# Performance work log

Hardware: AMD Instinct MI355X
Metric: run time of the kernel (lower is better)

## Reference

```python
import jax, jax.numpy as jnp
import numpy as np

N_HEAD_HALF = 8          # config.n_head // 2
LAMBDA_INIT = 0.2        # diff_lambda_init
RMS_EPS = 1.1920929e-07  # torch.finfo(float32).eps (F.rms_norm default)
ROPE_BASE = 10000.0


def setup_inputs() -> dict:
    key = jax.random.key(0)
    ks = jax.random.split(key, 9)
    B, T, C = 2, 2048, 2048
    HD = C // N_HEAD_HALF  # 256
    s = 0.02
    return {
        "x": jax.random.normal(ks[0], (B, T, C), jnp.float32),
        "wq": jax.random.normal(ks[1], (C, C), jnp.float32) * s,
        "wk": jax.random.normal(ks[2], (C, C), jnp.float32) * s,
        "wv": jax.random.normal(ks[3], (C, C), jnp.float32) * s,
        "wo": jax.random.normal(ks[4], (C, C), jnp.float32) * s,
        "lq1": jax.random.normal(ks[5], (HD,), jnp.float32) * 0.1,
        "lk1": jax.random.normal(ks[6], (HD,), jnp.float32) * 0.1,
        "lq2": jax.random.normal(ks[7], (HD,), jnp.float32) * 0.1,
        "lk2": jax.random.normal(ks[8], (HD,), jnp.float32) * 0.1,
    }


def _rms_norm(x):
    var = jnp.mean(x * x, axis=-1, keepdims=True)
    return x * jax.lax.rsqrt(var + RMS_EPS)


def _rotary(x):
    # Faithful to original bug: positions run along axis 1 (the HEAD axis),
    # since Rotary is applied after transpose(1,2). x: (B, NH, T, D)
    d = x.shape[-1]
    inv_freq = (1.0 / ROPE_BASE) ** (jnp.arange(0, d, 2, dtype=jnp.float32) / d)
    t = jnp.arange(x.shape[1], dtype=jnp.float32)
    freqs = jnp.outer(t, inv_freq)                      # (NH, d/2)
    cos = jnp.cos(freqs)[None, :, None, :]
    sin = jnp.sin(freqs)[None, :, None, :]
    x1, x2 = jnp.split(x, 2, axis=-1)
    return jnp.concatenate((x1 * cos + x2 * sin, -x1 * sin + x2 * cos), axis=-1)


def _causal_attn(q, k, v, scale):
    # q,k: (B,NH,T,Dh)  v: (B,NH,T,HD)
    T = q.shape[2]
    s = jnp.einsum("bhqd,bhkd->bhqk", q, k) * scale
    mask = jnp.tril(jnp.ones((T, T), dtype=bool))
    s = jnp.where(mask, s, jnp.float32(-jnp.inf))
    p = jax.nn.softmax(s, axis=-1)
    return jnp.einsum("bhqk,bhkd->bhqd", p, v)


def reference(x, wq, wk, wv, wo, lq1, lk1, lq2, lk2):
    B, T, C = x.shape
    NH = N_HEAD_HALF
    HD = C // NH
    HH = HD // 2

    lam1 = jnp.exp(jnp.sum(lq1 * lk1))
    lam2 = jnp.exp(jnp.sum(lq2 * lk2))
    lam = lam1 - lam2 + LAMBDA_INIT

    q = (x @ wq.T).reshape(B, T, NH, 2, HH).transpose(0, 2, 1, 3, 4)
    k = (x @ wk.T).reshape(B, T, NH, 2, HH).transpose(0, 2, 1, 3, 4)
    v = (x @ wv.T).reshape(B, T, NH, HD).transpose(0, 2, 1, 3)

    q1 = _rotary(_rms_norm(q[..., 0, :]))
    q2 = _rotary(_rms_norm(q[..., 1, :]))
    k1 = _rotary(_rms_norm(k[..., 0, :]))
    k2 = _rotary(_rms_norm(k[..., 1, :]))

    scale = 1.0 / jnp.sqrt(jnp.float32(HH))
    y = _causal_attn(q1, k1, v, scale) - lam * _causal_attn(q2, k2, v, scale)

    y = y.transpose(0, 2, 1, 3).reshape(B, T, C)
    y = (y @ wo.T) * (1.0 - LAMBDA_INIT)
    return y
```

## Files before the change

### kernel.cpp

```cpp
#include <hip/hip_runtime.h>
#include <hip/hip_bf16.h>

using bf16 = __hip_bfloat16;
typedef __bf16 bf16x8_t __attribute__((ext_vector_type(8)));
typedef __bf16 bf16x4_t __attribute__((ext_vector_type(4)));
typedef float f32x4  __attribute__((ext_vector_type(4)));
typedef float f32x16 __attribute__((ext_vector_type(16)));

#define AS1 __attribute__((address_space(1)))
#define AS3 __attribute__((address_space(3)))

__device__ __forceinline__ void gll16(const void* g, void* l) {
  __builtin_amdgcn_global_load_lds((const AS1 void*)g, (AS3 void*)l, 16u, 0, 0u);
}

__device__ __forceinline__ __bf16 tobf(float f) {
  bf16 h = __float2bfloat16(f);
  return __builtin_bit_cast(__bf16, h);
}

__global__ __launch_bounds__(256) void k_cvt(
    const float* __restrict__ x,  const float* __restrict__ wq,
    const float* __restrict__ wk, const float* __restrict__ wv,
    const float* __restrict__ wo,
    bf16* __restrict__ xb,  bf16* __restrict__ wqb, bf16* __restrict__ wkb,
    bf16* __restrict__ wvb, bf16* __restrict__ wob) {
  size_t id = (size_t)blockIdx.x * 256 + threadIdx.x;
  const float* s; bf16* d; size_t off;
  if (id < 2097152) { s = x; d = xb; off = id; }
  else {
    size_t r = id - 2097152;
    unsigned w = (unsigned)(r >> 20);
    off = r & 1048575u;
    s = (w == 0) ? wq : (w == 1) ? wk : (w == 2) ? wv : wo;
    d = (w == 0) ? wqb : (w == 1) ? wkb : (w == 2) ? wvb : wob;
  }
  const float4 v = ((const float4*)s)[off];
  bf16x4_t o = { tobf(v.x), tobf(v.y), tobf(v.z), tobf(v.w) };
  *(bf16x4_t*)(d + off * 4) = o;
}

__global__ __launch_bounds__(256) void k_lam(
    const float* __restrict__ lq1, const float* __restrict__ lk1,
    const float* __restrict__ lq2, const float* __restrict__ lk2,
    float* __restrict__ lam) {
  __shared__ float r1[4], r2[4];
  int t = threadIdx.x;
  float a = lq1[t] * lk1[t];
  float b = lq2[t] * lk2[t];
#pragma unroll
  for (int s = 1; s < 64; s <<= 1) { a += __shfl_xor(a, s); b += __shfl_xor(b, s); }
  if ((t & 63) == 0) { r1[t >> 6] = a; r2[t >> 6] = b; }
  __syncthreads();
  if (t == 0) {
    float s1 = r1[0] + r1[1] + r1[2] + r1[3];
    float s2 = r2[0] + r2[1] + r2[2] + r2[3];
    *lam = expf(s1) - expf(s2) + 0.2f;
  }
}

#define MFMA16(a, b, c) __builtin_amdgcn_mfma_f32_16x16x32_bf16(a, b, c, 0, 0, 0)

template<bool SWAP>
__device__ __forceinline__ void gemm256(
    const bf16* __restrict__ A, const bf16* __restrict__ B,
    int m0, int n0, bf16* lds, f32x4 (&acc)[8][4]) {
  const int tid = threadIdx.x, lane = tid & 63;
  const int wave = tid >> 6, m = wave >> 2, n = wave & 3;
  const int g = lane >> 4, l15 = lane & 15, l7 = lane & 7;

  const int sid0 = tid, sid1 = tid + 512;
  const int sr0 = sid0 >> 3, sc0 = (sid0 & 7) ^ (sr0 & 7);
  const int sr1 = sid1 >> 3, sc1 = (sid1 & 7) ^ (sr1 & 7);

  auto stageA = [&](int t, int h) {
    bf16* d = lds + ((size_t)((t & 1) * 2 + h)) * 8192;
    gll16(A + (size_t)(m0 + h * 128 + sr0) * 2048 + t * 64 + sc0 * 8, d + sid0 * 8);
    gll16(A + (size_t)(m0 + h * 128 + sr1) * 2048 + t * 64 + sc1 * 8, d + sid1 * 8);
  };
  auto stageB = [&](int t, int h) {
    bf16* d = lds + 32768 + ((size_t)((t & 1) * 2 + h)) * 8192;
    gll16(B + (size_t)(n0 + h * 128 + sr0) * 2048 + t * 64 + sc0 * 8, d + sid0 * 8);
    gll16(B + (size_t)(n0 + h * 128 + sr1) * 2048 + t * 64 + sc1 * 8, d + sid1 * 8);
  };

  stageA(0, 0); stageB(0, 0); stageB(0, 1); stageA(0, 1);
  stageA(1, 0); stageB(1, 0); stageB(1, 1);
  asm volatile("s_waitcnt vmcnt(6)\n\ts_barrier" ::: "memory");

  for (int t = 0; t < 32; ++t) {
    const bf16* lA0 = lds + ((size_t)((t & 1) * 2 + 0)) * 8192;
    const bf16* lA1 = lds + ((size_t)((t & 1) * 2 + 1)) * 8192;
    const bf16* lB0 = lds + 32768 + ((size_t)((t & 1) * 2 + 0)) * 8192;
    const bf16* lB1 = lds + 32768 + ((size_t)((t & 1) * 2 + 1)) * 8192;
    bf16x8_t afl[4][2], afh[4][2], bvl[2][2], bvh[2][2];

#pragma unroll
    for (int ks = 0; ks < 2; ++ks) {
      const int pc = ((ks * 4 + g) ^ l7) * 8;
#pragma unroll
      for (int rf = 0; rf < 4; ++rf)
        afl[rf][ks] = *(const bf16x8_t*)(lA0 + (m * 64 + rf * 16 + l15) * 64 + pc);
#pragma unroll
      for (int cf = 0; cf < 2; ++cf)
        bvl[cf][ks] = *(const bf16x8_t*)(lB0 + (cf * 64 + n * 16 + l15) * 64 + pc);
    }
    if (t + 1 < 32) stageA(t + 1, 1);
    asm volatile("s_barrier" ::: "memory");
    __builtin_amdgcn_s_setprio(1);
#pragma unroll
    for (int ks = 0; ks < 2; ++ks)
#pragma unroll
      for (int rf = 0; rf < 4; ++rf)
#pragma unroll
        for (int cf = 0; cf < 2; ++cf)
          acc[rf][cf] = SWAP ? MFMA16(bvl[cf][ks], afl[rf][ks], acc[rf][cf])
                             : MFMA16(afl[rf][ks], bvl[cf][ks], acc[rf][cf]);
    __builtin_amdgcn_s_setprio(0);
    asm volatile("s_barrier" ::: "memory");

#pragma unroll
    for (int ks = 0; ks < 2; ++ks) {
      const int pc = ((ks * 4 + g) ^ l7) * 8;
#pragma unroll
      for (int cf = 0; cf < 2; ++cf)
        bvh[cf][ks] = *(const bf16x8_t*)(lB1 + (cf * 64 + n * 16 + l15) * 64 + pc);
    }
    if (t + 2 < 32) stageA(t + 2, 0);
    asm volatile("s_barrier" ::: "memory");
    __builtin_amdgcn_s_setprio(1);
#pragma unroll
    for (int ks = 0; ks < 2; ++ks)
#pragma unroll
      for (int rf = 0; rf < 4; ++rf)
#pragma unroll
        for (int cf = 0; cf < 2; ++cf)
          acc[rf][cf + 2] = SWAP ? MFMA16(bvh[cf][ks], afl[rf][ks], acc[rf][cf + 2])
                                 : MFMA16(afl[rf][ks], bvh[cf][ks], acc[rf][cf + 2]);
    __builtin_amdgcn_s_setprio(0);
    asm volatile("s_barrier" ::: "memory");

#pragma unroll
    for (int ks = 0; ks < 2; ++ks) {
      const int pc = ((ks * 4 + g) ^ l7) * 8;
#pragma unroll
      for (int rf = 0; rf < 4; ++rf)
        afh[rf][ks] = *(const bf16x8_t*)(lA1 + (m * 64 + rf * 16 + l15) * 64 + pc);
    }
    if (t + 2 < 32) stageB(t + 2, 0);
    asm volatile("s_barrier" ::: "memory");
    __builtin_amdgcn_s_setprio(1);
#pragma unroll
    for (int ks = 0; ks < 2; ++ks)
#pragma unroll
      for (int rf = 0; rf < 4; ++rf)
#pragma unroll
        for (int cf = 0; cf < 2; ++cf)
          acc[rf + 4][cf + 2] = SWAP ? MFMA16(bvh[cf][ks], afh[rf][ks], acc[rf + 4][cf + 2])
                                     : MFMA16(afh[rf][ks], bvh[cf][ks], acc[rf + 4][cf + 2]);
    __builtin_amdgcn_s_setprio(0);
    asm volatile("s_barrier" ::: "memory");

    if (t + 2 < 32) stageB(t + 2, 1);
    asm volatile("s_barrier" ::: "memory");
    __builtin_amdgcn_s_setprio(1);
#pragma unroll
    for (int ks = 0; ks < 2; ++ks)
#pragma unroll
      for (int rf = 0; rf < 4; ++rf)
#pragma unroll
        for (int cf = 0; cf < 2; ++cf)
          acc[rf + 4][cf] = SWAP ? MFMA16(bvl[cf][ks], afh[rf][ks], acc[rf + 4][cf])
                                 : MFMA16(afh[rf][ks], bvl[cf][ks], acc[rf + 4][cf]);
    __builtin_amdgcn_s_setprio(0);
    if (t < 30)      asm volatile("s_waitcnt vmcnt(6)\n\ts_barrier" ::: "memory");
    else             asm volatile("s_waitcnt vmcnt(0)\n\ts_barrier" ::: "memory");
  }
}

__global__ __launch_bounds__(512, 2) void k_gemm_qkv(
    const bf16* __restrict__ xb,
    const bf16* __restrict__ wqb, const bf16* __restrict__ wkb,
    const bf16* __restrict__ wvb,
    bf16* __restrict__ q1, bf16* __restrict__ q2,
    bf16* __restrict__ k1, bf16* __restrict__ k2,
    bf16* __restrict__ vt) {
  __shared__ __align__(16) bf16 lds[65536];
  __shared__ float exs[2][4][256];
  __shared__ float lCs[64], lSn[64];
  const int z  = blockIdx.z;
  const int m0 = blockIdx.y * 256, n0 = blockIdx.x * 256;
  const int nh = blockIdx.x;
  const int tid = threadIdx.x, lane = tid & 63, wave = tid >> 6;
  const int m = wave >> 2, n = wave & 3;
  const int g = lane >> 4, l15 = lane & 15;
  f32x4 acc[8][4] = {};

  if (z < 2) {
    if (tid < 64) {
      float fr = exp2f(-(float)tid * 0.20762050593045951f);
      float sn, cs;
      sincosf((float)nh * fr, &sn, &cs);
      lCs[tid] = cs; lSn[tid] = sn;
    }
    const bf16* Bm = z ? wkb : wqb;
    gemm256<true>(xb, Bm, m0, n0, lds, acc);

#pragma unroll
    for (int rf = 0; rf < 8; ++rf) {
      float s0 = 0.f, s1 = 0.f;
#pragma unroll
      for (int r = 0; r < 4; ++r) {
        s0 += acc[rf][0][r] * acc[rf][0][r] + acc[rf][1][r] * acc[rf][1][r];
        s1 += acc[rf][2][r] * acc[rf][2][r] + acc[rf][3][r] * acc[rf][3][r];
      }
      s0 += __shfl_xor(s0, 16); s0 += __shfl_xor(s0, 32);
      s1 += __shfl_xor(s1, 16); s1 += __shfl_xor(s1, 32);
      const int rrow = (rf >> 2) * 128 + m * 64 + (rf & 3) * 16 + l15;
      if (g == 0) { exs[0][n][rrow] = s0; exs[1][n][rrow] = s1; }
    }
    __syncthreads();
    bf16* dst1 = z ? k1 : q1;
    bf16* dst2 = z ? k2 : q2;
    const int j = n * 16 + 4 * g;
#pragma unroll
    for (int rf = 0; rf < 8; ++rf) {
      const int rrow = (rf >> 2) * 128 + m * 64 + (rf & 3) * 16 + l15;
      const float t0 = exs[0][0][rrow] + exs[0][1][rrow] + exs[0][2][rrow] + exs[0][3][rrow];
      const float t1 = exs[1][0][rrow] + exs[1][1][rrow] + exs[1][2][rrow] + exs[1][3][rrow];
      const float inv0 = rsqrtf(t0 * (1.0f / 128.0f) + 1.1920929e-07f);
      const float inv1 = rsqrtf(t1 * (1.0f / 128.0f) + 1.1920929e-07f);
      const size_t base = ((size_t)(m0 + rrow) * 8 + nh) * 128;
      bf16x4_t o1a, o2a, o1b, o2b;
#pragma unroll
      for (int r = 0; r < 4; ++r) {
        const float cs = lCs[j + r], sn = lSn[j + r];
        float x1 = acc[rf][0][r] * inv0, x2 = acc[rf][1][r] * inv0;
        o1a[r] = tobf(x1 * cs + x2 * sn);
        o2a[r] = tobf(x2 * cs - x1 * sn);
        x1 = acc[rf][2][r] * inv1; x2 = acc[rf][3][r] * inv1;
        o1b[r] = tobf(x1 * cs + x2 * sn);
        o2b[r] = tobf(x2 * cs - x1 * sn);
      }
      *(bf16x4_t*)(dst1 + base + j)      = o1a;
      *(bf16x4_t*)(dst1 + base + j + 64) = o2a;
      *(bf16x4_t*)(dst2 + base + j)      = o1b;
      *(bf16x4_t*)(dst2 + base + j + 64) = o2b;
    }
  } else {
    gemm256<false>(xb, wvb, m0, n0, lds, acc);
#pragma unroll
    for (int rf = 0; rf < 8; ++rf)
#pragma unroll
      for (int cf = 0; cf < 4; ++cf) {
        const int rb = m0 + (rf >> 2) * 128 + m * 64 + (rf & 3) * 16 + 4 * g;
        const int hd = (cf & 1) * 64 + (cf >> 1) * 128 + n * 16 + l15;
        const int b = rb >> 11, t = rb & 2047;
        bf16x4_t pv;
#pragma unroll
        for (int r = 0; r < 4; ++r) pv[r] = tobf(acc[rf][cf][r]);
        *(bf16x4_t*)(vt + ((size_t)((b * 8 + nh) * 256 + hd)) * 2048 + t) = pv;
      }
  }
}

template<bool SWAP>
__device__ __forceinline__ void gemm_core(
    const bf16* __restrict__ A, const bf16* __restrict__ Bm,
    int m0, int n0, bf16* lA, bf16* lB, f32x4 (&acc)[4][4]) {
  const int tid  = threadIdx.x;
  const int lane = tid & 63;
  const int g    = lane >> 4;
  const int l15  = lane & 15;
  const int l7   = lane & 7;
  const int wave = tid >> 6;
  const int wm   = (wave >> 1) * 64;
  const int wn   = (wave & 1) * 64;

  int srow[4], ssc[4];
#pragma unroll
  for (int j = 0; j < 4; ++j) {
    int id = tid + j * 256;
    srow[j] = id >> 3;
    ssc[j]  = (id & 7) ^ (srow[j] & 7);
  }

  for (int k0 = 0; k0 < 2048; k0 += 64) {
    __syncthreads();
#pragma unroll
    for (int j = 0; j < 4; ++j) {
      int id = tid + j * 256;
      gll16(A  + (size_t)(m0 + srow[j]) * 2048 + k0 + ssc[j] * 8, lA + id * 8);
      gll16(Bm + (size_t)(n0 + srow[j]) * 2048 + k0 + ssc[j] * 8, lB + id * 8);
    }
    __syncthreads();
#pragma unroll
    for (int ks = 0; ks < 2; ++ks) {
      const int pc = (ks * 4 + g) ^ l7;
      bf16x8_t af[4], bfr[4];
#pragma unroll
      for (int mt = 0; mt < 4; ++mt)
        af[mt] = *(const bf16x8_t*)(lA + (wm + mt * 16 + l15) * 64 + pc * 8);
#pragma unroll
      for (int nt = 0; nt < 4; ++nt)
        bfr[nt] = *(const bf16x8_t*)(lB + (wn + nt * 16 + l15) * 64 + pc * 8);
#pragma unroll
      for (int mt = 0; mt < 4; ++mt)
#pragma unroll
        for (int nt = 0; nt < 4; ++nt) {
          if (SWAP)
            acc[mt][nt] = MFMA16(bfr[nt], af[mt], acc[mt][nt]);
          else
            acc[mt][nt] = MFMA16(af[mt], bfr[nt], acc[mt][nt]);
        }
    }
  }
}

__global__ __launch_bounds__(256) void k_gemm_out(
    const bf16* __restrict__ yb, const bf16* __restrict__ wob,
    float* __restrict__ outp) {
  __shared__ __align__(16) bf16 lA[128 * 64];
  __shared__ __align__(16) bf16 lB[128 * 64];
  const int m0 = blockIdx.y * 128, n0 = blockIdx.x * 128;
  f32x4 acc[4][4] = {};
  gemm_core<true>(yb, wob, m0, n0, lA, lB, acc);
  const int lane = threadIdx.x & 63, wave = threadIdx.x >> 6;
  const int g = lane >> 4, l15 = lane & 15;
  const int wm = (wave >> 1) * 64, wn = (wave & 1) * 64;
#pragma unroll
  for (int mt = 0; mt < 4; ++mt)
#pragma unroll
    for (int nt = 0; nt < 4; ++nt) {
      int row = m0 + wm + mt * 16 + l15;
      int col = n0 + wn + nt * 16 + 4 * g;
      f32x4 v;
#pragma unroll
      for (int r = 0; r < 4; ++r) v[r] = acc[mt][nt][r] * 0.8f;
      *(f32x4*)(outp + (size_t)row * 2048 + col) = v;
    }
}

__global__ __launch_bounds__(512, 2) void k_flash(
    const bf16* __restrict__ q1b, const bf16* __restrict__ q2b,
    const bf16* __restrict__ k1b, const bf16* __restrict__ k2b,
    const bf16* __restrict__ vtb, const float* __restrict__ lamp,
    bf16* __restrict__ yb) {
  __shared__ __align__(16) bf16 smem[65536];
  __shared__ float mx[8][32], lx[8][32];
  const int tid  = threadIdx.x;
  const int lane = tid & 63, wave = tid >> 6;
  const int pair = blockIdx.x;
  const int bh = blockIdx.y;
  const int b = bh >> 3, nh = bh & 7;
  const int at = wave & 1, qg = (wave >> 1) & 1, kvh = wave >> 2;
  const int l31 = lane & 31, g5 = lane >> 5, l7 = lane & 7;
  const float sl2e = 0.12751743f;
  const float lam = *lamp;

  auto stage = [&](int kt, int buf) {
    bf16* dst = smem + buf * 32768;
    const int k0 = kt * 64;
#pragma unroll
    for (int it = 0; it < 2; ++it) {
      int id = tid + it * 512;
      int row = id >> 4, c = id & 15;
      int sc = (c & 8) | ((c & 7) ^ (row & 7));
      size_t goff = ((size_t)(b * 2048 + k0 + row) * 8 + nh) * 128 + sc * 8;
      gll16(k1b + goff, dst + id * 8);
      gll16(k2b + goff, dst + 8192 + id * 8);
    }
#pragma unroll
    for (int it = 0; it < 4; ++it) {
      int id = tid + it * 512;
      int row = id >> 3, c = id & 7;
      int sc = c ^ (row & 7);
      gll16(vtb + ((size_t)(bh * 256 + row)) * 2048 + k0 + sc * 8,
            dst + 16384 + id * 8);
    }
  };

  bf16x8_t qf[8];
  auto loadQ = [&](int qt) {
    int qglob = qt * 64 + qg * 32 + l31;
    const bf16* qp = (at ? q2b : q1b) +
                     ((size_t)(b * 2048 + qglob) * 8 + nh) * 128 + g5 * 8;
#pragma unroll
    for (int ks = 0; ks < 8; ++ks) qf[ks] = *(const bf16x8_t*)(qp + ks * 16);
  };

  f32x16 O[8];
  float mrun, lrun;
  auto resetO = [&]() {
#pragma unroll
    for (int i = 0; i < 8; ++i)
#pragma unroll
      for (int j = 0; j < 16; ++j) O[i][j] = 0.f;
    mrun = -1e30f; lrun = 0.f;
  };

  auto step = [&](int kt, int buf, int qt) {
    const int k0 = kt * 64 + kvh * 32;
    if (k0 > qt * 64 + qg * 32 + 31) return;
    const bf16* lk = smem + buf * 32768 + (at ? 8192 : 0);
    const bf16* lv = smem + buf * 32768 + 16384;
    const int qglob = qt * 64 + qg * 32 + l31;

    f32x16 s0;
#pragma unroll
    for (int j = 0; j < 16; ++j) s0[j] = 0.f;
#pragma unroll
    for (int ks = 0; ks < 8; ++ks) {
      int cl = ks * 2 + g5;
      int pc = (cl & 8) | ((cl & 7) ^ l7);
      bf16x8_t a0 = *(const bf16x8_t*)(lk + (kvh * 32 + l31) * 128 + pc * 8);
      s0 = __builtin_amdgcn_mfma_f32_32x32x16_bf16(a0, qf[ks], s0, 0, 0, 0);
    }

    const bool needmask = (k0 + 31 > qt * 64 + qg * 32);
    float rmax = -3.0e38f;
#pragma unroll
    for (int r = 0; r < 16; ++r) {
      float v0 = s0[r] * sl2e;
      if (needmask) {
        int key0 = k0 + (r & 3) + 8 * (r >> 2) + 4 * g5;
        if (key0 > qglob) v0 = -1e30f;
      }
      s0[r] = v0;
      rmax = fmaxf(rmax, v0);
    }
    rmax = fmaxf(rmax, __shfl_xor(rmax, 32));
    if (!__all(rmax - mrun <= 8.0f)) {
      float mnew = fmaxf(mrun, rmax);
      float alpha = exp2f(mrun - mnew);
      lrun *= alpha;
#pragma unroll
      for (int i = 0; i < 8; ++i) O[i] *= alpha;
      mrun = mnew;
    }
    float psum = 0.f;
#pragma unroll
    for (int r = 0; r < 16; ++r) {
      float p0 = exp2f(s0[r] - mrun);
      s0[r] = p0;
      psum += p0;
    }
    psum += __shfl_xor(psum, 32);
    lrun += psum;

#pragma unroll
    for (int sl = 0; sl < 2; ++sl) {
      bf16x4_t lo, hi;
#pragma unroll
      for (int j = 0; j < 4; ++j) {
        lo[j] = tobf(s0[sl * 8 + j]);
        hi[j] = tobf(s0[sl * 8 + 4 + j]);
      }
      bf16x4_t send = g5 ? lo : hi;
      int2 si = __builtin_bit_cast(int2, send);
      int2 ri;
      ri.x = __shfl_xor(si.x, 32);
      ri.y = __shfl_xor(si.y, 32);
      bf16x4_t recv = __builtin_bit_cast(bf16x4_t, ri);
      bf16x4_t f0 = g5 ? recv : lo;
      bf16x4_t f1 = g5 ? hi : recv;
      bf16x8_t pf = { f0[0], f0[1], f0[2], f0[3], f1[0], f1[1], f1[2], f1[3] };

      const int cl = kvh * 4 + sl * 2 + g5;
#pragma unroll
      for (int mt = 0; mt < 8; ++mt) {
        bf16x8_t vf = *(const bf16x8_t*)(lv + (mt * 32 + l31) * 64 + (cl ^ l7) * 8);
        O[mt] = __builtin_amdgcn_mfma_f32_32x32x16_bf16(vf, pf, O[mt], 0, 0, 0);
      }
    }
  };

  auto finish = [&](int qt, bf16* cbuf) {
    const int qglob = qt * 64 + qg * 32 + l31;
    float* XF = (float*)cbuf;
    __syncthreads();
    if (g5 == 0) { mx[wave][l31] = mrun; lx[wave][l31] = lrun; }
    __syncthreads();
    const float mo  = mx[wave ^ 4][l31];
    const float lo2 = lx[wave ^ 4][l31];
    const float ms = fmaxf(mrun, mo);
    const float ws = exp2f(mrun - ms);
    const float wo = exp2f(mo - ms);
    const float lstar = lrun * ws + lo2 * wo;
#pragma unroll
    for (int rnd = 0; rnd < 2; ++rnd) {
      if (at == rnd && kvh == 1) {
#pragma unroll
        for (int mt = 0; mt < 8; ++mt)
#pragma unroll
          for (int rq = 0; rq < 4; ++rq) {
            int hd = mt * 32 + 8 * rq + 4 * g5;
            f32x4 v;
#pragma unroll
            for (int i = 0; i < 4; ++i) v[i] = O[mt][rq * 4 + i] * ws;
            *(f32x4*)(XF + qg * 8192 + l31 * 256 + hd) = v;
          }
      }
      __syncthreads();
      if (at == rnd && kvh == 0) {
#pragma unroll
        for (int mt = 0; mt < 8; ++mt)
#pragma unroll
          for (int rq = 0; rq < 4; ++rq) {
            int hd = mt * 32 + 8 * rq + 4 * g5;
            f32x4 v = *(const f32x4*)(XF + qg * 8192 + l31 * 256 + hd);
#pragma unroll
            for (int i = 0; i < 4; ++i)
              O[mt][rq * 4 + i] = O[mt][rq * 4 + i] * ws + v[i];
          }
      }
      __syncthreads();
    }
    const float invl = 1.f / lstar;
    if (kvh == 0 && at == 1) {
      const float f = lam * invl;
#pragma unroll
      for (int mt = 0; mt < 8; ++mt)
#pragma unroll
        for (int rq = 0; rq < 4; ++rq) {
          int hd = mt * 32 + 8 * rq + 4 * g5;
          bf16x4_t pv;
#pragma unroll
          for (int i = 0; i < 4; ++i) pv[i] = tobf(O[mt][rq * 4 + i] * f);
          *(bf16x4_t*)(cbuf + (size_t)(qg * 32 + l31) * 264 + hd) = pv;
        }
    }
    __syncthreads();
    if (kvh == 0 && at == 0) {
#pragma unroll
      for (int mt = 0; mt < 8; ++mt)
#pragma unroll
        for (int rq = 0; rq < 4; ++rq) {
          int hd = mt * 32 + 8 * rq + 4 * g5;
          bf16x4_t o2 = *(const bf16x4_t*)(cbuf + (size_t)(qg * 32 + l31) * 264 + hd);
          bf16x4_t pv;
#pragma unroll
          for (int i = 0; i < 4; ++i)
            pv[i] = tobf(O[mt][rq * 4 + i] * invl - (float)o2[i]);
          *(bf16x4_t*)(yb + (size_t)(b * 2048 + qglob) * 2048 + nh * 256 + hd) = pv;
        }
    }
  };

  const int qtB = 31 - pair, qtA = pair;

  loadQ(qtB);
  resetO();
  stage(0, 0);
  for (int kt = 0; kt <= qtB; ++kt) {
    __syncthreads();
    if (kt < qtB) stage(kt + 1, (kt + 1) & 1);
    else          stage(0, (kt + 1) & 1);
    step(kt, kt & 1, qtB);
  }
  finish(qtB, smem + (qtB & 1) * 32768);

  loadQ(qtA);
  resetO();
  for (int kt = 0; kt <= qtA; ++kt) {
    __syncthreads();
    if (kt < qtA) stage(kt + 1, (qtB + kt + 2) & 1);
    step(kt, (qtB + 1 + kt) & 1, qtA);
  }
  finish(qtA, smem + 32768);
}

extern "C" void kernel_launch(void* const* d_in, const int* in_sizes, int n_in,
                              void* d_out, int out_size, void* d_ws, size_t ws_size,
                              hipStream_t stream) {
  (void)in_sizes; (void)n_in; (void)out_size; (void)ws_size;
  const float* x   = (const float*)d_in[0];
  const float* wq  = (const float*)d_in[1];
  const float* wk  = (const float*)d_in[2];
  const float* wv  = (const float*)d_in[3];
  const float* wo  = (const float*)d_in[4];
  const float* lq1 = (const float*)d_in[5];
  const float* lk1 = (const float*)d_in[6];
  const float* lq2 = (const float*)d_in[7];
  const float* lk2 = (const float*)d_in[8];
  float* out = (float*)d_out;

  char* p = (char*)d_ws;
  float* lam = (float*)p;            p += 256;
  bf16* xb  = (bf16*)p;              p += (size_t)4096 * 2048 * 2;
  bf16* wqb = (bf16*)p;              p += (size_t)2048 * 2048 * 2;
  bf16* wkb = (bf16*)p;              p += (size_t)2048 * 2048 * 2;
  bf16* wvb = (bf16*)p;              p += (size_t)2048 * 2048 * 2;
  bf16* wob = (bf16*)p;              p += (size_t)2048 * 2048 * 2;
  bf16* vt  = (bf16*)p;              p += (size_t)4096 * 2048 * 2;
  bf16* q1b = (bf16*)p;              p += (size_t)4096 * 1024 * 2;
  bf16* q2b = (bf16*)p;              p += (size_t)4096 * 1024 * 2;
  bf16* k1b = (bf16*)p;              p += (size_t)4096 * 1024 * 2;
  bf16* k2b = (bf16*)p;              p += (size_t)4096 * 1024 * 2;
  bf16* yb  = (bf16*)p;              p += (size_t)4096 * 2048 * 2;

  k_cvt<<<24576, 256, 0, stream>>>(x, wq, wk, wv, wo, xb, wqb, wkb, wvb, wob);
  k_lam<<<1, 256, 0, stream>>>(lq1, lk1, lq2, lk2, lam);
  k_gemm_qkv<<<dim3(8, 16, 3), 512, 0, stream>>>(xb, wqb, wkb, wvb,
                                                 q1b, q2b, k1b, k2b, vt);
  k_flash<<<dim3(16, 16), 512, 0, stream>>>(q1b, q2b, k1b, k2b, vt, lam, yb);
  k_gemm_out<<<dim3(16, 32), 256, 0, stream>>>(yb, wob, out);
}
```

Measured before the change: 425.7 us.

## Retile GEMMs to 256x128 with triple-buffered LDS pipeline and fuse lambda kernel

Replaces the 256x256 double-buffered QKV GEMM with a shared 256x128 tile GEMM that keeps three LDS stages and prefetches two k-steps ahead, doubling the QKV grid. The output projection, which used a simple 128x128 single-buffered GEMM, now uses the same pipelined 256x128 path. The lambda reduction moves into an extra block of the conversion kernel to drop one launch. The epilogue's RMS norm now sums across two waves through shared memory. The aim is more blocks in flight and better latency hiding, at the cost of less reuse per tile.

```diff
diff --git a/kernel.cpp b/kernel.cpp
--- a/kernel.cpp
+++ b/kernel.cpp
@@ -23,8 +23,26 @@
     const float* __restrict__ x,  const float* __restrict__ wq,
     const float* __restrict__ wk, const float* __restrict__ wv,
     const float* __restrict__ wo,
+    const float* __restrict__ lq1, const float* __restrict__ lk1,
+    const float* __restrict__ lq2, const float* __restrict__ lk2,
     bf16* __restrict__ xb,  bf16* __restrict__ wqb, bf16* __restrict__ wkb,
-    bf16* __restrict__ wvb, bf16* __restrict__ wob) {
+    bf16* __restrict__ wvb, bf16* __restrict__ wob, float* __restrict__ lam) {
+  if (blockIdx.x == 24576) {
+    __shared__ float r1[4], r2[4];
+    int t = threadIdx.x;
+    float a = lq1[t] * lk1[t];
+    float b = lq2[t] * lk2[t];
+#pragma unroll
+    for (int s = 1; s < 64; s <<= 1) { a += __shfl_xor(a, s); b += __shfl_xor(b, s); }
+    if ((t & 63) == 0) { r1[t >> 6] = a; r2[t >> 6] = b; }
+    __syncthreads();
+    if (t == 0) {
+      float s1 = r1[0] + r1[1] + r1[2] + r1[3];
+      float s2 = r2[0] + r2[1] + r2[2] + r2[3];
+      *lam = expf(s1) - expf(s2) + 0.2f;
+    }
+    return;
+  }
   size_t id = (size_t)blockIdx.x * 256 + threadIdx.x;
   const float* s; bf16* d; size_t off;
   if (id < 2097152) { s = x; d = xb; off = id; }
@@ -40,72 +58,82 @@
   *(bf16x4_t*)(d + off * 4) = o;
 }
 
-__global__ __launch_bounds__(256) void k_lam(
-    const float* __restrict__ lq1, const float* __restrict__ lk1,
-    const float* __restrict__ lq2, const float* __restrict__ lk2,
-    float* __restrict__ lam) {
-  __shared__ float r1[4], r2[4];
-  int t = threadIdx.x;
-  float a = lq1[t] * lk1[t];
-  float b = lq2[t] * lk2[t];
-#pragma unroll
-  for (int s = 1; s < 64; s <<= 1) { a += __shfl_xor(a, s); b += __shfl_xor(b, s); }
-  if ((t & 63) == 0) { r1[t >> 6] = a; r2[t >> 6] = b; }
-  __syncthreads();
-  if (t == 0) {
-    float s1 = r1[0] + r1[1] + r1[2] + r1[3];
-    float s2 = r2[0] + r2[1] + r2[2] + r2[3];
-    *lam = expf(s1) - expf(s2) + 0.2f;
-  }
-}
-
 #define MFMA16(a, b, c) __builtin_amdgcn_mfma_f32_16x16x32_bf16(a, b, c, 0, 0, 0)
 
 template<bool SWAP>
-__device__ __forceinline__ void gemm256(
+__device__ __forceinline__ void gemmKS(
     const bf16* __restrict__ A, const bf16* __restrict__ B,
-    int m0, int n0, bf16* lds, f32x4 (&acc)[8][4]) {
+    int m0, int n0, bf16* lA_, bf16* lB_, f32x4 (&acc)[4][4]) {
   const int tid = threadIdx.x, lane = tid & 63;
-  const int wave = tid >> 6, m = wave >> 2, n = wave & 3;
+  const int wave = tid >> 6, m = wave >> 1, n = wave & 1;
   const int g = lane >> 4, l15 = lane & 15, l7 = lane & 7;
 
-  const int sid0 = tid, sid1 = tid + 512;
-  const int sr0 = sid0 >> 3, sc0 = (sid0 & 7) ^ (sr0 & 7);
-  const int sr1 = sid1 >> 3, sc1 = (sid1 & 7) ^ (sr1 & 7);
-
-  auto stageA = [&](int t, int h) {
-    bf16* d = lds + ((size_t)((t & 1) * 2 + h)) * 8192;
-    gll16(A + (size_t)(m0 + h * 128 + sr0) * 2048 + t * 64 + sc0 * 8, d + sid0 * 8);
-    gll16(A + (size_t)(m0 + h * 128 + sr1) * 2048 + t * 64 + sc1 * 8, d + sid1 * 8);
-  };
-  auto stageB = [&](int t, int h) {
-    bf16* d = lds + 32768 + ((size_t)((t & 1) * 2 + h)) * 8192;
-    gll16(B + (size_t)(n0 + h * 128 + sr0) * 2048 + t * 64 + sc0 * 8, d + sid0 * 8);
-    gll16(B + (size_t)(n0 + h * 128 + sr1) * 2048 + t * 64 + sc1 * 8, d + sid1 * 8);
-  };
-
-  stageA(0, 0); stageB(0, 0); stageB(0, 1); stageA(0, 1);
-  stageA(1, 0); stageB(1, 0); stageB(1, 1);
+  auto stageA = [&](int t, int sl) {
+    bf16* d = lA_ + sl * 16384;
+#pragma unroll
+    for (int j = 0; j < 4; ++j) {
+      int id = tid + j * 512;
+      int row = id >> 3, sc = (id & 7) ^ (row & 7);
+      gll16(A + (size_t)(m0 + row) * 2048 + t * 64 + sc * 8, d + id * 8);
+    }
+  };
+  auto stageB = [&](int t, int sl) {
+    bf16* d = lB_ + sl * 8192;
+#pragma unroll
+    for (int j = 0; j < 2; ++j) {
+      int id = tid + j * 512;
+      int row = id >> 3, sc = (id & 7) ^ (row & 7);
+      gll16(B + (size_t)(n0 + row) * 2048 + t * 64 + sc * 8, d + id * 8);
+    }
+  };
+
+  stageA(0, 0); stageB(0, 0); stageA(1, 1); stageB(1, 1);
   asm volatile("s_waitcnt vmcnt(6)\n\ts_barrier" ::: "memory");
 
+  int s = 0;
   for (int t = 0; t < 32; ++t) {
-    const bf16* lA0 = lds + ((size_t)((t & 1) * 2 + 0)) * 8192;
-    const bf16* lA1 = lds + ((size_t)((t & 1) * 2 + 1)) * 8192;
-    const bf16* lB0 = lds + 32768 + ((size_t)((t & 1) * 2 + 0)) * 8192;
-    const bf16* lB1 = lds + 32768 + ((size_t)((t & 1) * 2 + 1)) * 8192;
-    bf16x8_t afl[4][2], afh[4][2], bvl[2][2], bvh[2][2];
+    const bf16* la = lA_ + s * 16384;
+    const bf16* lb = lB_ + s * 8192;
+    int sp = s + 2; if (sp >= 3) sp -= 3;
+    bf16x8_t af[4][2], bv[4][2];
 
 #pragma unroll
     for (int ks = 0; ks < 2; ++ks) {
       const int pc = ((ks * 4 + g) ^ l7) * 8;
 #pragma unroll
       for (int rf = 0; rf < 4; ++rf)
-        afl[rf][ks] = *(const bf16x8_t*)(lA0 + (m * 64 + rf * 16 + l15) * 64 + pc);
+        af[rf][ks] = *(const bf16x8_t*)(la + (m * 64 + rf * 16 + l15) * 64 + pc);
 #pragma unroll
       for (int cf = 0; cf < 2; ++cf)
-        bvl[cf][ks] = *(const bf16x8_t*)(lB0 + (cf * 64 + n * 16 + l15) * 64 + pc);
-    }
-    if (t + 1 < 32) stageA(t + 1, 1);
+        bv[cf][ks] = *(const bf16x8_t*)(lb + (n * 32 + cf * 16 + l15) * 64 + pc);
+    }
+    if (t + 2 < 32) stageA(t + 2, sp);
+    asm volatile("s_barrier" ::: "memory");
+#pragma unroll
+    for (int ks = 0; ks < 2; ++ks) {
+      const int pc = ((ks * 4 + g) ^ l7) * 8;
+#pragma unroll
+      for (int cf = 0; cf < 2; ++cf)
+        bv[cf + 2][ks] =
+            *(const bf16x8_t*)(lb + (n * 32 + cf * 16 + 64 + l15) * 64 + pc);
+    }
+    __builtin_amdgcn_s_setprio(1);
+#pragma unroll
+    for (int ks = 0; ks < 2; ++ks)
+#pragma unroll
+      for (int rf = 0; rf < 4; ++rf)
+#pragma unroll
+        for (int cf = 0; cf < 2; ++cf)
+          acc[rf][cf] = SWAP ? MFMA16(bv[cf][ks], af[rf][ks], acc[rf][cf])
+                             : MFMA16(af[rf][ks], bv[cf][ks], acc[rf][cf]);
+    __builtin_amdgcn_s_setprio(0);
+
+    if (t + 2 < 32) {
+      stageB(t + 2, sp);
+      asm volatile("s_waitcnt vmcnt(6)" ::: "memory");
+    } else if (t == 30) {
+      asm volatile("s_waitcnt vmcnt(0)" ::: "memory");
+    }
     asm volatile("s_barrier" ::: "memory");
     __builtin_amdgcn_s_setprio(1);
 #pragma unroll
@@ -114,67 +142,10 @@
       for (int rf = 0; rf < 4; ++rf)
 #pragma unroll
         for (int cf = 0; cf < 2; ++cf)
-          acc[rf][cf] = SWAP ? MFMA16(bvl[cf][ks], afl[rf][ks], acc[rf][cf])
-                             : MFMA16(afl[rf][ks], bvl[cf][ks], acc[rf][cf]);
+          acc[rf][cf + 2] = SWAP ? MFMA16(bv[cf + 2][ks], af[rf][ks], acc[rf][cf + 2])
+                                 : MFMA16(af[rf][ks], bv[cf + 2][ks], acc[rf][cf + 2]);
     __builtin_amdgcn_s_setprio(0);
-    asm volatile("s_barrier" ::: "memory");
-
-#pragma unroll
-    for (int ks = 0; ks < 2; ++ks) {
-      const int pc = ((ks * 4 + g) ^ l7) * 8;
-#pragma unroll
-      for (int cf = 0; cf < 2; ++cf)
-        bvh[cf][ks] = *(const bf16x8_t*)(lB1 + (cf * 64 + n * 16 + l15) * 64 + pc);
-    }
-    if (t + 2 < 32) stageA(t + 2, 0);
-    asm volatile("s_barrier" ::: "memory");
-    __builtin_amdgcn_s_setprio(1);
-#pragma unroll
-    for (int ks = 0; ks < 2; ++ks)
-#pragma unroll
-      for (int rf = 0; rf < 4; ++rf)
-#pragma unroll
-        for (int cf = 0; cf < 2; ++cf)
-          acc[rf][cf + 2] = SWAP ? MFMA16(bvh[cf][ks], afl[rf][ks], acc[rf][cf + 2])
-                                 : MFMA16(afl[rf][ks], bvh[cf][ks], acc[rf][cf + 2]);
-    __builtin_amdgcn_s_setprio(0);
-    asm volatile("s_barrier" ::: "memory");
-
-#pragma unroll
-    for (int ks = 0; ks < 2; ++ks) {
-      const int pc = ((ks * 4 + g) ^ l7) * 8;
-#pragma unroll
-      for (int rf = 0; rf < 4; ++rf)
-        afh[rf][ks] = *(const bf16x8_t*)(lA1 + (m * 64 + rf * 16 + l15) * 64 + pc);
-    }
-    if (t + 2 < 32) stageB(t + 2, 0);
-    asm volatile("s_barrier" ::: "memory");
-    __builtin_amdgcn_s_setprio(1);
-#pragma unroll
-    for (int ks = 0; ks < 2; ++ks)
-#pragma unroll
-      for (int rf = 0; rf < 4; ++rf)
-#pragma unroll
-        for (int cf = 0; cf < 2; ++cf)
-          acc[rf + 4][cf + 2] = SWAP ? MFMA16(bvh[cf][ks], afh[rf][ks], acc[rf + 4][cf + 2])
-                                     : MFMA16(afh[rf][ks], bvh[cf][ks], acc[rf + 4][cf + 2]);
-    __builtin_amdgcn_s_setprio(0);
-    asm volatile("s_barrier" ::: "memory");
-
-    if (t + 2 < 32) stageB(t + 2, 1);
-    asm volatile("s_barrier" ::: "memory");
-    __builtin_amdgcn_s_setprio(1);
-#pragma unroll
-    for (int ks = 0; ks < 2; ++ks)
-#pragma unroll
-      for (int rf = 0; rf < 4; ++rf)
-#pragma unroll
-        for (int cf = 0; cf < 2; ++cf)
-          acc[rf + 4][cf] = SWAP ? MFMA16(bvl[cf][ks], afh[rf][ks], acc[rf + 4][cf])
-                                 : MFMA16(afh[rf][ks], bvl[cf][ks], acc[rf + 4][cf]);
-    __builtin_amdgcn_s_setprio(0);
-    if (t < 30)      asm volatile("s_waitcnt vmcnt(6)\n\ts_barrier" ::: "memory");
-    else             asm volatile("s_waitcnt vmcnt(0)\n\ts_barrier" ::: "memory");
+    s = (s == 2) ? 0 : s + 1;
   }
 }
 
@@ -185,16 +156,17 @@
     bf16* __restrict__ q1, bf16* __restrict__ q2,
     bf16* __restrict__ k1, bf16* __restrict__ k2,
     bf16* __restrict__ vt) {
-  __shared__ __align__(16) bf16 lds[65536];
-  __shared__ float exs[2][4][256];
+  __shared__ __align__(16) bf16 lA[3 * 16384];
+  __shared__ __align__(16) bf16 lB[3 * 8192];
+  __shared__ float exs[2][256];
   __shared__ float lCs[64], lSn[64];
   const int z  = blockIdx.z;
-  const int m0 = blockIdx.y * 256, n0 = blockIdx.x * 256;
-  const int nh = blockIdx.x;
+  const int m0 = blockIdx.y * 256, n0 = blockIdx.x * 128;
+  const int nh = blockIdx.x >> 1, p = blockIdx.x & 1;
   const int tid = threadIdx.x, lane = tid & 63, wave = tid >> 6;
-  const int m = wave >> 2, n = wave & 3;
+  const int m = wave >> 1, n = wave & 1;
   const int g = lane >> 4, l15 = lane & 15;
-  f32x4 acc[8][4] = {};
+  f32x4 acc[4][4] = {};
 
   if (z < 2) {
     if (tid < 64) {
@@ -204,57 +176,54 @@
       lCs[tid] = cs; lSn[tid] = sn;
     }
     const bf16* Bm = z ? wkb : wqb;
-    gemm256<true>(xb, Bm, m0, n0, lds, acc);
-
-#pragma unroll
-    for (int rf = 0; rf < 8; ++rf) {
-      float s0 = 0.f, s1 = 0.f;
-#pragma unroll
-      for (int r = 0; r < 4; ++r) {
-        s0 += acc[rf][0][r] * acc[rf][0][r] + acc[rf][1][r] * acc[rf][1][r];
-        s1 += acc[rf][2][r] * acc[rf][2][r] + acc[rf][3][r] * acc[rf][3][r];
-      }
-      s0 += __shfl_xor(s0, 16); s0 += __shfl_xor(s0, 32);
-      s1 += __shfl_xor(s1, 16); s1 += __shfl_xor(s1, 32);
-      const int rrow = (rf >> 2) * 128 + m * 64 + (rf & 3) * 16 + l15;
-      if (g == 0) { exs[0][n][rrow] = s0; exs[1][n][rrow] = s1; }
-    }
-    __syncthreads();
-    bf16* dst1 = z ? k1 : q1;
-    bf16* dst2 = z ? k2 : q2;
-    const int j = n * 16 + 4 * g;
-#pragma unroll
-    for (int rf = 0; rf < 8; ++rf) {
-      const int rrow = (rf >> 2) * 128 + m * 64 + (rf & 3) * 16 + l15;
-      const float t0 = exs[0][0][rrow] + exs[0][1][rrow] + exs[0][2][rrow] + exs[0][3][rrow];
-      const float t1 = exs[1][0][rrow] + exs[1][1][rrow] + exs[1][2][rrow] + exs[1][3][rrow];
-      const float inv0 = rsqrtf(t0 * (1.0f / 128.0f) + 1.1920929e-07f);
-      const float inv1 = rsqrtf(t1 * (1.0f / 128.0f) + 1.1920929e-07f);
+    gemmKS<true>(xb, Bm, m0, n0, lA, lB, acc);
+
+    float ssr[4];
+#pragma unroll
+    for (int rf = 0; rf < 4; ++rf) {
+      float ss = 0.f;
+#pragma unroll
+      for (int cf = 0; cf < 4; ++cf)
+#pragma unroll
+        for (int r = 0; r < 4; ++r) ss += acc[rf][cf][r] * acc[rf][cf][r];
+      ss += __shfl_xor(ss, 16);
+      ss += __shfl_xor(ss, 32);
+      ssr[rf] = ss;
+      if (g == 0) exs[n][m * 64 + rf * 16 + l15] = ss;
+    }
+    __syncthreads();
+    bf16* dst = z ? (p ? k2 : k1) : (p ? q2 : q1);
+#pragma unroll
+    for (int rf = 0; rf < 4; ++rf) {
+      const int rrow = m * 64 + rf * 16 + l15;
+      const float tt = ssr[rf] + exs[n ^ 1][rrow];
+      const float inv = rsqrtf(tt * (1.0f / 128.0f) + 1.1920929e-07f);
       const size_t base = ((size_t)(m0 + rrow) * 8 + nh) * 128;
-      bf16x4_t o1a, o2a, o1b, o2b;
-#pragma unroll
-      for (int r = 0; r < 4; ++r) {
-        const float cs = lCs[j + r], sn = lSn[j + r];
-        float x1 = acc[rf][0][r] * inv0, x2 = acc[rf][1][r] * inv0;
-        o1a[r] = tobf(x1 * cs + x2 * sn);
-        o2a[r] = tobf(x2 * cs - x1 * sn);
-        x1 = acc[rf][2][r] * inv1; x2 = acc[rf][3][r] * inv1;
-        o1b[r] = tobf(x1 * cs + x2 * sn);
-        o2b[r] = tobf(x2 * cs - x1 * sn);
-      }
-      *(bf16x4_t*)(dst1 + base + j)      = o1a;
-      *(bf16x4_t*)(dst1 + base + j + 64) = o2a;
-      *(bf16x4_t*)(dst2 + base + j)      = o1b;
-      *(bf16x4_t*)(dst2 + base + j + 64) = o2b;
+#pragma unroll
+      for (int cf = 0; cf < 2; ++cf) {
+        const int jb = n * 32 + cf * 16 + 4 * g;
+        bf16x4_t o1v, o2v;
+#pragma unroll
+        for (int r = 0; r < 4; ++r) {
+          const float cs = lCs[jb + r], sn = lSn[jb + r];
+          float x1 = acc[rf][cf][r] * inv;
+          float x2 = acc[rf][cf + 2][r] * inv;
+          o1v[r] = tobf(x1 * cs + x2 * sn);
+          o2v[r] = tobf(x2 * cs - x1 * sn);
+        }
+        *(bf16x4_t*)(dst + base + jb)      = o1v;
+        *(bf16x4_t*)(dst + base + jb + 64) = o2v;
+      }
     }
   } else {
-    gemm256<false>(xb, wvb, m0, n0, lds, acc);
-#pragma unroll
-    for (int rf = 0; rf < 8; ++rf)
+    gemmKS<false>(xb, wvb, m0, n0, lA, lB, acc);
+#pragma unroll
+    for (int rf = 0; rf < 4; ++rf)
 #pragma unroll
       for (int cf = 0; cf < 4; ++cf) {
-        const int rb = m0 + (rf >> 2) * 128 + m * 64 + (rf & 3) * 16 + 4 * g;
-        const int hd = (cf & 1) * 64 + (cf >> 1) * 128 + n * 16 + l15;
+        const int rb = m0 + m * 64 + rf * 16 + 4 * g;
+        const int col = n0 + n * 32 + (cf & 1) * 16 + (cf >> 1) * 64 + l15;
+        const int hd = col & 255;
         const int b = rb >> 11, t = rb & 2047;
         bf16x4_t pv;
 #pragma unroll
@@ -264,79 +233,26 @@
   }
 }
 
-template<bool SWAP>
-__device__ __forceinline__ void gemm_core(
-    const bf16* __restrict__ A, const bf16* __restrict__ Bm,
-    int m0, int n0, bf16* lA, bf16* lB, f32x4 (&acc)[4][4]) {
-  const int tid  = threadIdx.x;
-  const int lane = tid & 63;
-  const int g    = lane >> 4;
-  const int l15  = lane & 15;
-  const int l7   = lane & 7;
-  const int wave = tid >> 6;
-  const int wm   = (wave >> 1) * 64;
-  const int wn   = (wave & 1) * 64;
-
-  int srow[4], ssc[4];
-#pragma unroll
-  for (int j = 0; j < 4; ++j) {
-    int id = tid + j * 256;
-    srow[j] = id >> 3;
-    ssc[j]  = (id & 7) ^ (srow[j] & 7);
-  }
-
-  for (int k0 = 0; k0 < 2048; k0 += 64) {
-    __syncthreads();
-#pragma unroll
-    for (int j = 0; j < 4; ++j) {
-      int id = tid + j * 256;
-      gll16(A  + (size_t)(m0 + srow[j]) * 2048 + k0 + ssc[j] * 8, lA + id * 8);
-      gll16(Bm + (size_t)(n0 + srow[j]) * 2048 + k0 + ssc[j] * 8, lB + id * 8);
-    }
-    __syncthreads();
-#pragma unroll
-    for (int ks = 0; ks < 2; ++ks) {
-      const int pc = (ks * 4 + g) ^ l7;
-      bf16x8_t af[4], bfr[4];
-#pragma unroll
-      for (int mt = 0; mt < 4; ++mt)
-        af[mt] = *(const bf16x8_t*)(lA + (wm + mt * 16 + l15) * 64 + pc * 8);
-#pragma unroll
-      for (int nt = 0; nt < 4; ++nt)
-        bfr[nt] = *(const bf16x8_t*)(lB + (wn + nt * 16 + l15) * 64 + pc * 8);
-#pragma unroll
-      for (int mt = 0; mt < 4; ++mt)
-#pragma unroll
-        for (int nt = 0; nt < 4; ++nt) {
-          if (SWAP)
-            acc[mt][nt] = MFMA16(bfr[nt], af[mt], acc[mt][nt]);
-          else
-            acc[mt][nt] = MFMA16(af[mt], bfr[nt], acc[mt][nt]);
-        }
-    }
-  }
-}
-
-__global__ __launch_bounds__(256) void k_gemm_out(
+__global__ __launch_bounds__(512, 2) void k_gemm_out(
     const bf16* __restrict__ yb, const bf16* __restrict__ wob,
     float* __restrict__ outp) {
-  __shared__ __align__(16) bf16 lA[128 * 64];
-  __shared__ __align__(16) bf16 lB[128 * 64];
-  const int m0 = blockIdx.y * 128, n0 = blockIdx.x * 128;
+  __shared__ __align__(16) bf16 lA[3 * 16384];
+  __shared__ __align__(16) bf16 lB[3 * 8192];
+  const int m0 = blockIdx.y * 256, n0 = blockIdx.x * 128;
+  const int tid = threadIdx.x, lane = tid & 63, wave = tid >> 6;
+  const int m = wave >> 1, n = wave & 1;
+  const int g = lane >> 4, l15 = lane & 15;
   f32x4 acc[4][4] = {};
-  gemm_core<true>(yb, wob, m0, n0, lA, lB, acc);
-  const int lane = threadIdx.x & 63, wave = threadIdx.x >> 6;
-  const int g = lane >> 4, l15 = lane & 15;
-  const int wm = (wave >> 1) * 64, wn = (wave & 1) * 64;
-#pragma unroll
-  for (int mt = 0; mt < 4; ++mt)
-#pragma unroll
-    for (int nt = 0; nt < 4; ++nt) {
-      int row = m0 + wm + mt * 16 + l15;
-      int col = n0 + wn + nt * 16 + 4 * g;
+  gemmKS<true>(yb, wob, m0, n0, lA, lB, acc);
+#pragma unroll
+  for (int rf = 0; rf < 4; ++rf)
+#pragma unroll
+    for (int cf = 0; cf < 4; ++cf) {
+      const int row = m0 + m * 64 + rf * 16 + l15;
+      const int col = n0 + n * 32 + (cf & 1) * 16 + (cf >> 1) * 64 + 4 * g;
       f32x4 v;
 #pragma unroll
-      for (int r = 0; r < 4; ++r) v[r] = acc[mt][nt][r] * 0.8f;
+      for (int r = 0; r < 4; ++r) v[r] = acc[rf][cf][r] * 0.8f;
       *(f32x4*)(outp + (size_t)row * 2048 + col) = v;
     }
 }
@@ -599,10 +515,10 @@
   bf16* k2b = (bf16*)p;              p += (size_t)4096 * 1024 * 2;
   bf16* yb  = (bf16*)p;              p += (size_t)4096 * 2048 * 2;
 
-  k_cvt<<<24576, 256, 0, stream>>>(x, wq, wk, wv, wo, xb, wqb, wkb, wvb, wob);
-  k_lam<<<1, 256, 0, stream>>>(lq1, lk1, lq2, lk2, lam);
-  k_gemm_qkv<<<dim3(8, 16, 3), 512, 0, stream>>>(xb, wqb, wkb, wvb,
-                                                 q1b, q2b, k1b, k2b, vt);
+  k_cvt<<<24577, 256, 0, stream>>>(x, wq, wk, wv, wo, lq1, lk1, lq2, lk2,
+                                   xb, wqb, wkb, wvb, wob, lam);
+  k_gemm_qkv<<<dim3(16, 16, 3), 512, 0, stream>>>(xb, wqb, wkb, wvb,
+                                                  q1b, q2b, k1b, k2b, vt);
   k_flash<<<dim3(16, 16), 512, 0, stream>>>(q1b, q2b, k1b, k2b, vt, lam, yb);
-  k_gemm_out<<<dim3(16, 32), 256, 0, stream>>>(yb, wob, out);
-}
+  k_gemm_out<<<dim3(16, 16), 512, 0, stream>>>(yb, wob, out);
+}
```

New measurement: 418.0 us. Within noise of the previous version (-1.8%).
